# Kernel tuning notes

Measured on AMD Instinct MI355X. Metric: run time of the kernel, lower is better.

Reference implementation:

```python
import jax, jax.numpy as jnp
import numpy as np

B, S, H, A = 32, 4096, 512, 256

def setup_inputs() -> dict:
    key = jax.random.key(0)
    ks = jax.random.split(key, 8)
    sH = 1.0 / np.sqrt(H)
    sA = 1.0 / np.sqrt(A)
    return {
        "encoder_outputs": jax.random.normal(ks[0], (B, S, H), dtype=jnp.float32),
        "decoder_hidden": jax.random.normal(ks[1], (B, H), dtype=jnp.float32),
        "W_enc": jax.random.uniform(ks[2], (H, A), jnp.float32, -sH, sH),
        "b_enc": jax.random.uniform(ks[3], (A,), jnp.float32, -sH, sH),
        "W_dec": jax.random.uniform(ks[4], (H, A), jnp.float32, -sH, sH),
        "b_dec": jax.random.uniform(ks[5], (A,), jnp.float32, -sH, sH),
        "W_e": jax.random.uniform(ks[6], (A,), jnp.float32, -sA, sA),
        "b_e": jax.random.uniform(ks[7], (), jnp.float32, -sA, sA),
    }

def reference(encoder_outputs, decoder_hidden, W_enc, b_enc, W_dec, b_dec, W_e, b_e):
    # [B,S,A] encoder projection
    enc_p = jnp.einsum('bsh,ha->bsa', encoder_outputs, W_enc) + b_enc
    # [B,1,A] decoder projection broadcast over S
    dec_p = (decoder_hidden @ W_dec + b_dec)[:, None, :]
    scores = jnp.einsum('bsa,a->bs', jnp.tanh(enc_p + dec_p), W_e) + b_e  # [B,S]
    attn = jax.nn.softmax(scores, axis=1)                                 # [B,S]
    context = jnp.einsum('bs,bsh->bh', attn, encoder_outputs)             # [B,H]
    return context, attn
```

## Files before the change

### kernel.cpp

```cpp
#include <hip/hip_runtime.h>
#include <hip/hip_bf16.h>
#include <stdint.h>


typedef __attribute__((ext_vector_type(4))) float f32x4;
typedef __attribute__((ext_vector_type(8))) short short8;

#define B_  32
#define S_  4096
#define H_  512
#define A_  256
#define CHUNKS_ 64

#define WS_WT     0
#define WS_BIAS   262144
#define WS_SCORES 294912
#define WS_M      819200
#define WS_L      827392
#define WS_PART   835584

#define STRIDE_ 520

static __device__ __forceinline__ short f2bf(float f) {
  union { float f; uint32_t u; } v; v.f = f;
  uint32_t r = (v.u + 0x7FFFu + ((v.u >> 16) & 1u)) >> 16;
  return (short)(uint16_t)r;
}
static __device__ __forceinline__ float bf2f(uint32_t lo16) {
  union { uint32_t u; float f; } v; v.u = lo16 << 16; return v.f;
}

__global__ __launch_bounds__(256) void prep_kernel(
    const float* __restrict__ dh, const float* __restrict__ W_enc,
    const float* __restrict__ b_enc, const float* __restrict__ W_dec,
    const float* __restrict__ b_dec, unsigned short* __restrict__ WT,
    float* __restrict__ bias) {
  __shared__ float dh_s[512];
  __shared__ unsigned short tile[64 * 66];
  const int tid = threadIdx.x;
  if (blockIdx.x < 32) {
    const int b = blockIdx.x;
    dh_s[tid]       = dh[(size_t)b * H_ + tid];
    dh_s[tid + 256] = dh[(size_t)b * H_ + tid + 256];
    __syncthreads();
    float s[4] = {0.f, 0.f, 0.f, 0.f};
    for (int k = 0; k < H_; k += 32) {
      #pragma unroll
      for (int j = 0; j < 32; ++j)
        s[j & 3] = fmaf(dh_s[k + j], W_dec[(size_t)(k + j) * A_ + tid], s[j & 3]);
    }
    bias[b * A_ + tid] = s[0] + s[1] + s[2] + s[3] + b_enc[tid] + b_dec[tid];
  } else {
    const int t = blockIdx.x - 32;
    const int kt = t >> 2, nt2 = t & 3;
    #pragma unroll
    for (int i = 0; i < 16; ++i) {
      int idx = tid + i * 256;
      int kk = idx >> 6, nn = idx & 63;
      tile[kk * 66 + nn] =
          (unsigned short)f2bf(W_enc[(size_t)(kt * 64 + kk) * A_ + nt2 * 64 + nn]);
    }
    __syncthreads();
    #pragma unroll
    for (int i = 0; i < 16; ++i) {
      int idx = tid + i * 256;
      int nn = idx >> 6, kk = idx & 63;
      WT[(size_t)(nt2 * 64 + nn) * H_ + kt * 64 + kk] = tile[kk * 66 + nn];
    }
  }
}

__global__ __launch_bounds__(256, 2) void fused_kernel(
    const float* __restrict__ enc, const unsigned short* __restrict__ WT,
    const float* __restrict__ bias, const float* __restrict__ We,
    float* __restrict__ scores, float* __restrict__ wsm,
    float* __restrict__ wsl, float* __restrict__ part) {
  __shared__ __align__(16) unsigned short stash[64 * STRIDE_];
  __shared__ float s_ps[4][64];
  __shared__ float s_e[64];

  const int tid = threadIdx.x, w = tid >> 6, lane = tid & 63;
  const int lm = lane & 15, lq = lane >> 4;
  const int b = blockIdx.x >> 6;
  const int chunk = blockIdx.x & 63;
  const int srow0 = blockIdx.x * 64;

  f32x4 acc[4][4];
  #pragma unroll
  for (int mt = 0; mt < 4; ++mt)
    #pragma unroll
    for (int nt = 0; nt < 4; ++nt)
      acc[mt][nt] = (f32x4){0.f, 0.f, 0.f, 0.f};

  const int arow = tid >> 2, akoff = (tid & 3) * 8;
  const float* aptr = enc + (size_t)(srow0 + arow) * H_ + akoff;
  unsigned short* swp = &stash[arow * STRIDE_ + akoff];

  const unsigned short* bptr = WT + (size_t)((w * 4) * 16 + lm) * H_ + lq * 8;

  short8 Bring[3][4];
  float4 abuf0_a, abuf0_b, abuf1_a, abuf1_b;

  abuf0_a = *(const float4*)aptr;
  abuf0_b = *(const float4*)(aptr + 4);
  {
    short8 sv;
    sv[0] = f2bf(abuf0_a.x); sv[1] = f2bf(abuf0_a.y); sv[2] = f2bf(abuf0_a.z); sv[3] = f2bf(abuf0_a.w);
    sv[4] = f2bf(abuf0_b.x); sv[5] = f2bf(abuf0_b.y); sv[6] = f2bf(abuf0_b.z); sv[7] = f2bf(abuf0_b.w);
    *(short8*)swp = sv;
  }
  abuf1_a = *(const float4*)(aptr + 32);
  abuf1_b = *(const float4*)(aptr + 36);
  #pragma unroll
  for (int j = 0; j < 4; ++j) {
    Bring[0][j] = *(const short8*)(bptr + (size_t)j * 16 * H_);
    Bring[1][j] = *(const short8*)(bptr + (size_t)j * 16 * H_ + 32);
  }
  __syncthreads();

  #pragma unroll
  for (int k = 0; k < 16; ++k) {
    const int kel = k * 32;
    float4 na_a, na_b;
    if (k + 2 < 16) {
      na_a = *(const float4*)(aptr + (k + 2) * 32);
      na_b = *(const float4*)(aptr + (k + 2) * 32 + 4);
    }
    if (k + 2 < 16) {
      #pragma unroll
      for (int j = 0; j < 4; ++j)
        Bring[(k + 2) % 3][j] = *(const short8*)(bptr + (size_t)j * 16 * H_ + (k + 2) * 32);
    }
    #pragma unroll
    for (int mt = 0; mt < 4; ++mt) {
      short8 af = *(const short8*)&stash[(mt * 16 + lm) * STRIDE_ + kel + lq * 8];
      #pragma unroll
      for (int j = 0; j < 4; ++j)
        acc[mt][j] = __builtin_amdgcn_mfma_f32_16x16x32_bf16(af, Bring[k % 3][j], acc[mt][j], 0, 0, 0);
    }
    if (k < 15) {
      float4 ca = (k & 1) ? abuf0_a : abuf1_a;
      float4 cb = (k & 1) ? abuf0_b : abuf1_b;
      short8 sv;
      sv[0] = f2bf(ca.x); sv[1] = f2bf(ca.y); sv[2] = f2bf(ca.z); sv[3] = f2bf(ca.w);
      sv[4] = f2bf(cb.x); sv[5] = f2bf(cb.y); sv[6] = f2bf(cb.z); sv[7] = f2bf(cb.w);
      *(short8*)(swp + (k + 1) * 32) = sv;
    }
    if (k + 2 < 16) {
      if (k & 1) { abuf1_a = na_a; abuf1_b = na_b; }
      else       { abuf0_a = na_a; abuf0_b = na_b; }
    }
    __syncthreads();
  }

  float psum[4][4] = {{0,0,0,0},{0,0,0,0},{0,0,0,0},{0,0,0,0}};
  #pragma unroll
  for (int j = 0; j < 4; ++j) {
    const int col = (w * 4 + j) * 16 + lm;
    const float dp = bias[b * A_ + col];
    const float wv = We[col];
    #pragma unroll
    for (int mt = 0; mt < 4; ++mt)
      #pragma unroll
      for (int r = 0; r < 4; ++r) {
        float x = acc[mt][j][r] + dp;
        float e = __expf(2.0f * x);
        float t = 1.0f - 2.0f * __builtin_amdgcn_rcpf(e + 1.0f);
        psum[mt][r] = fmaf(t, wv, psum[mt][r]);
      }
  }
  #pragma unroll
  for (int o = 1; o < 16; o <<= 1)
    #pragma unroll
    for (int mt = 0; mt < 4; ++mt)
      #pragma unroll
      for (int r = 0; r < 4; ++r)
        psum[mt][r] += __shfl_xor(psum[mt][r], o, 64);
  if (lm == 0) {
    #pragma unroll
    for (int mt = 0; mt < 4; ++mt)
      #pragma unroll
      for (int r = 0; r < 4; ++r)
        s_ps[w][mt * 16 + lq * 4 + r] = psum[mt][r];
  }
  __syncthreads();

  if (tid < 64) {
    const float sc = s_ps[0][tid] + s_ps[1][tid] + s_ps[2][tid] + s_ps[3][tid];
    scores[srow0 + tid] = sc;
    float m = sc;
    #pragma unroll
    for (int o = 1; o < 64; o <<= 1) m = fmaxf(m, __shfl_xor(m, o, 64));
    const float e = __expf(sc - m);
    float l = e;
    #pragma unroll
    for (int o = 1; o < 64; o <<= 1) l += __shfl_xor(l, o, 64);
    s_e[tid] = e;
    if (tid == 0) {
      wsm[b * CHUNKS_ + chunk] = m;
      wsl[b * CHUNKS_ + chunk] = l;
    }
  }
  __syncthreads();

  float cx0 = 0.f, cx1 = 0.f;
  #pragma unroll 8
  for (int row = 0; row < 64; ++row) {
    uint32_t pv = *(const uint32_t*)&stash[row * STRIDE_ + (tid << 1)];
    float wr = s_e[row];
    cx0 = fmaf(wr, bf2f(pv & 0xffffu), cx0);
    cx1 = fmaf(wr, bf2f(pv >> 16), cx1);
  }
  float2 o2; o2.x = cx0; o2.y = cx1;
  *(float2*)&part[(size_t)(b * CHUNKS_ + chunk) * H_ + (tid << 1)] = o2;
}

__global__ __launch_bounds__(256) void finalize_kernel(
    const float* __restrict__ scores, const float* __restrict__ wsm,
    const float* __restrict__ wsl, const float* __restrict__ part,
    float* __restrict__ ctx, float* __restrict__ attn) {
  __shared__ float wgt[CHUNKS_];
  __shared__ float s_ml[2];
  const int b = blockIdx.x, tid = threadIdx.x;
  if (tid < 64) {
    float mc = wsm[b * CHUNKS_ + tid];
    float lc = wsl[b * CHUNKS_ + tid];
    float M = mc;
    #pragma unroll
    for (int o = 1; o < 64; o <<= 1) M = fmaxf(M, __shfl_xor(M, o, 64));
    float wv = __expf(mc - M);
    float Lp = wv * lc;
    #pragma unroll
    for (int o = 1; o < 64; o <<= 1) Lp += __shfl_xor(Lp, o, 64);
    wgt[tid] = wv;
    if (tid == 0) { s_ml[0] = M; s_ml[1] = Lp; }
  }
  __syncthreads();
  const float M = s_ml[0];
  const float invL = 1.0f / s_ml[1];

  #pragma unroll
  for (int hh = 0; hh < 2; ++hh) {
    const int h = tid + hh * 256;
    float s = 0.f;
    #pragma unroll 8
    for (int c = 0; c < CHUNKS_; ++c)
      s = fmaf(wgt[c], part[(size_t)(b * CHUNKS_ + c) * H_ + h], s);
    ctx[(size_t)b * H_ + h] = s * invL;
  }
  #pragma unroll
  for (int i = 0; i < 16; ++i) {
    const int s_ = tid + i * 256;
    attn[(size_t)b * S_ + s_] = __expf(scores[(size_t)b * S_ + s_] - M) * invL;
  }
}

extern "C" void kernel_launch(void* const* d_in, const int* in_sizes, int n_in,
                              void* d_out, int out_size, void* d_ws, size_t ws_size,
                              hipStream_t stream) {
  const float* enc   = (const float*)d_in[0];
  const float* dh    = (const float*)d_in[1];
  const float* W_enc = (const float*)d_in[2];
  const float* b_enc = (const float*)d_in[3];
  const float* W_dec = (const float*)d_in[4];
  const float* b_dec = (const float*)d_in[5];
  const float* W_e   = (const float*)d_in[6];

  char* ws = (char*)d_ws;
  unsigned short* WT = (unsigned short*)(ws + WS_WT);
  float* bias   = (float*)(ws + WS_BIAS);
  float* scores = (float*)(ws + WS_SCORES);
  float* wsm    = (float*)(ws + WS_M);
  float* wsl    = (float*)(ws + WS_L);
  float* part   = (float*)(ws + WS_PART);

  float* ctx  = (float*)d_out;
  float* attn = (float*)d_out + B_ * H_;

  prep_kernel<<<dim3(64), dim3(256), 0, stream>>>(dh, W_enc, b_enc, W_dec, b_dec, WT, bias);
  fused_kernel<<<dim3(2048), dim3(256), 0, stream>>>(enc, WT, bias, W_e, scores, wsm, wsl, part);
  finalize_kernel<<<dim3(32), dim3(256), 0, stream>>>(scores, wsm, wsl, part, ctx, attn);
}
```

Measured before the change: 419.3 us.

## Load whole encoder tile up front and drop per-k barriers in GEMM loop

Each thread now issues all 16 of its encoder-row float4 pairs at once and converts the whole 64x512 tile to bf16 in LDS. A single barrier follows, and the MFMA loop then runs with no __syncthreads per k-step. This trades the software-pipelined double-buffer for maximal memory-level parallelism and fewer barriers. The cost is 128 extra VGPRs of staging, which may pressure the launch_bounds(256,2) occupancy target or cause spills. It also loses overlap between the global loads and the MFMA work.

```diff
diff --git a/kernel.cpp b/kernel.cpp
--- a/kernel.cpp
+++ b/kernel.cpp
@@ -85,72 +85,57 @@
   const int chunk = blockIdx.x & 63;
   const int srow0 = blockIdx.x * 64;
 
-  f32x4 acc[4][4];
-  #pragma unroll
-  for (int mt = 0; mt < 4; ++mt)
-    #pragma unroll
-    for (int nt = 0; nt < 4; ++nt)
-      acc[mt][nt] = (f32x4){0.f, 0.f, 0.f, 0.f};
-
-  const int arow = tid >> 2, akoff = (tid & 3) * 8;
-  const float* aptr = enc + (size_t)(srow0 + arow) * H_ + akoff;
-  unsigned short* swp = &stash[arow * STRIDE_ + akoff];
+  const int arow = tid >> 2, akq = (tid & 3) * 8;
+  const float* aptr = enc + (size_t)(srow0 + arow) * H_ + akq;
+  unsigned short* swp = &stash[arow * STRIDE_ + akq];
 
   const unsigned short* bptr = WT + (size_t)((w * 4) * 16 + lm) * H_ + lq * 8;
 
+  float4 buf[16][2];
+  #pragma unroll
+  for (int k = 0; k < 16; ++k) {
+    buf[k][0] = *(const float4*)(aptr + k * 32);
+    buf[k][1] = *(const float4*)(aptr + k * 32 + 4);
+  }
   short8 Bring[3][4];
-  float4 abuf0_a, abuf0_b, abuf1_a, abuf1_b;
-
-  abuf0_a = *(const float4*)aptr;
-  abuf0_b = *(const float4*)(aptr + 4);
-  {
-    short8 sv;
-    sv[0] = f2bf(abuf0_a.x); sv[1] = f2bf(abuf0_a.y); sv[2] = f2bf(abuf0_a.z); sv[3] = f2bf(abuf0_a.w);
-    sv[4] = f2bf(abuf0_b.x); sv[5] = f2bf(abuf0_b.y); sv[6] = f2bf(abuf0_b.z); sv[7] = f2bf(abuf0_b.w);
-    *(short8*)swp = sv;
-  }
-  abuf1_a = *(const float4*)(aptr + 32);
-  abuf1_b = *(const float4*)(aptr + 36);
   #pragma unroll
   for (int j = 0; j < 4; ++j) {
     Bring[0][j] = *(const short8*)(bptr + (size_t)j * 16 * H_);
     Bring[1][j] = *(const short8*)(bptr + (size_t)j * 16 * H_ + 32);
   }
-  __syncthreads();
-
   #pragma unroll
   for (int k = 0; k < 16; ++k) {
-    const int kel = k * 32;
-    float4 na_a, na_b;
+    short8 sv;
+    sv[0] = f2bf(buf[k][0].x); sv[1] = f2bf(buf[k][0].y);
+    sv[2] = f2bf(buf[k][0].z); sv[3] = f2bf(buf[k][0].w);
+    sv[4] = f2bf(buf[k][1].x); sv[5] = f2bf(buf[k][1].y);
+    sv[6] = f2bf(buf[k][1].z); sv[7] = f2bf(buf[k][1].w);
+    *(short8*)(swp + k * 32) = sv;
+  }
+  __syncthreads();
+
+  f32x4 acc[4][4];
+  #pragma unroll
+  for (int mt = 0; mt < 4; ++mt)
+    #pragma unroll
+    for (int j = 0; j < 4; ++j)
+      acc[mt][j] = (f32x4){0.f, 0.f, 0.f, 0.f};
+
+  #pragma unroll
+  for (int k = 0; k < 16; ++k) {
     if (k + 2 < 16) {
-      na_a = *(const float4*)(aptr + (k + 2) * 32);
-      na_b = *(const float4*)(aptr + (k + 2) * 32 + 4);
-    }
-    if (k + 2 < 16) {
       #pragma unroll
       for (int j = 0; j < 4; ++j)
-        Bring[(k + 2) % 3][j] = *(const short8*)(bptr + (size_t)j * 16 * H_ + (k + 2) * 32);
+        Bring[(k + 2) % 3][j] =
+            *(const short8*)(bptr + (size_t)j * 16 * H_ + (k + 2) * 32);
     }
     #pragma unroll
     for (int mt = 0; mt < 4; ++mt) {
-      short8 af = *(const short8*)&stash[(mt * 16 + lm) * STRIDE_ + kel + lq * 8];
+      short8 af = *(const short8*)&stash[(mt * 16 + lm) * STRIDE_ + k * 32 + lq * 8];
       #pragma unroll
       for (int j = 0; j < 4; ++j)
         acc[mt][j] = __builtin_amdgcn_mfma_f32_16x16x32_bf16(af, Bring[k % 3][j], acc[mt][j], 0, 0, 0);
     }
-    if (k < 15) {
-      float4 ca = (k & 1) ? abuf0_a : abuf1_a;
-      float4 cb = (k & 1) ? abuf0_b : abuf1_b;
-      short8 sv;
-      sv[0] = f2bf(ca.x); sv[1] = f2bf(ca.y); sv[2] = f2bf(ca.z); sv[3] = f2bf(ca.w);
-      sv[4] = f2bf(cb.x); sv[5] = f2bf(cb.y); sv[6] = f2bf(cb.z); sv[7] = f2bf(cb.w);
-      *(short8*)(swp + (k + 1) * 32) = sv;
-    }
-    if (k + 2 < 16) {
-      if (k & 1) { abuf1_a = na_a; abuf1_b = na_b; }
-      else       { abuf0_a = na_a; abuf0_b = na_b; }
-    }
-    __syncthreads();
   }
 
   float psum[4][4] = {{0,0,0,0},{0,0,0,0},{0,0,0,0},{0,0,0,0}};
```

Measured after the change: 430.5 us. +2.7%, slower.
